# Kernel tuning notes

Measured on AMD Instinct MI355X. Metric: run time of the kernel, lower is better.

The kernel has to match this reference:

```python
import jax, jax.numpy as jnp
import numpy as np

B, D, E = 128, 1024, 1024   # batch, word_rnn_size, word_encoding_size
NV, NL = 36, 20             # visual regions, language memory slots
T = 4                       # max_att_step
EPS = 0.01                  # opt.epsilon
SCALE = 0.02


def _lstm_cell(x, h, c, Wih, Whh, bih, bhh):
    # torch.nn.LSTMCell gate order: i, f, g, o
    g = x @ Wih.T + bih + h @ Whh.T + bhh
    i, f, gg, o = jnp.split(g, 4, axis=-1)
    c2 = jax.nn.sigmoid(f) * c + jax.nn.sigmoid(i) * jnp.tanh(gg)
    h2 = jax.nn.sigmoid(o) * jnp.tanh(c2)
    return h2, c2


def _kv_attention(h_att, vkey, vval, lkey, lval, kvs):
    # stand-in for the externally-passed kv_attention module:
    # scaled dot-product attention over visual and language memories
    q = h_att + kvs                                   # [B,D]
    inv = 1.0 / np.sqrt(D)
    va = jax.nn.softmax(jnp.einsum('bnd,bd->bn', vkey, q) * inv, axis=-1)
    vctx = jnp.einsum('bn,bnd->bd', va, vval)
    la = jax.nn.softmax(jnp.einsum('bmd,bd->bm', lkey, q) * inv, axis=-1)
    lctx = jnp.einsum('bm,bmd->bd', la, lval)
    return vctx, lctx, jnp.tanh(kvs + vctx + lctx)


def _update_kv(out, vkey, lkey):
    # stand-in for the externally-passed update_kv module
    return vkey + 0.01 * out[:, None, :], lkey + 0.01 * out[:, None, :]


def _forward(xt, fc_feats, visual_value, visual_key, lang_value, lang_key,
             kv_state, state_h, state_c,
             att_Wih, att_Whh, att_bih, att_bhh,
             lang_Wih, lang_Whh, lang_bih, lang_bhh,
             conf_W1, conf_b1, conf_W2, conf_b2,
             it, max_att_step):
    word_exist = (it > 0).astype(jnp.float32)         # [B]
    prev_h = state_h[-1]
    # att_lstm input is constant across halting steps (state is not updated in the loop)
    att_in = jnp.concatenate([prev_h, fc_feats, xt], axis=1)  # [B, E+2D]
    z1 = jnp.zeros((B, 1), jnp.float32)
    zD = jnp.zeros((B, D), jnp.float32)
    zB = jnp.zeros((B,), jnp.float32)
    carry0 = (z1, jnp.ones((B, 1), jnp.float32), zD, zD, zD, zD, zD, zB,
              visual_key, lang_key, kv_state)

    def body(carry, i):
        accum, sel, hA, cA, hL, cL, outA, cost, vkey, lkey, kvs = carry
        h_att, c_att = _lstm_cell(att_in, state_h[0], state_c[0],
                                  att_Wih, att_Whh, att_bih, att_bhh)
        vctx, lctx, kvs = _kv_attention(h_att, vkey, visual_value, lkey, lang_value, kvs)
        lang_in = jnp.concatenate([vctx, lctx, h_att], axis=1)  # [B,3D]
        h_lang, c_lang = _lstm_cell(lang_in, state_h[1], state_c[1],
                                    lang_Wih, lang_Whh, lang_bih, lang_bhh)
        out = h_lang  # F.dropout in eval mode is identity
        vkey, lkey = _update_kv(out, vkey, lkey)
        # confidence MLP: Linear -> ReLU -> Linear -> Sigmoid
        p = jax.nn.sigmoid(jax.nn.relu(h_lang @ conf_W1.T + conf_b1) @ conf_W2.T + conf_b2)  # [B,1]
        beta = p * (1.0 - accum)
        accum = accum + beta * sel
        hA = hA + beta * h_att * sel
        cA = cA + beta * c_att * sel
        hL = hL + beta * h_lang * sel
        cL = cL + beta * c_lang * sel
        outA = outA + beta * out * sel
        cost = cost + (i + 1.0) * (1.0 - p[:, 0]) * sel[:, 0]
        sel = jax.lax.stop_gradient((accum < 1.0 - EPS).astype(jnp.float32)) * sel
        return (accum, sel, hA, cA, hL, cL, outA, cost, vkey, lkey, kvs), None

    carry, _ = jax.lax.scan(body, carry0, jnp.arange(max_att_step, dtype=jnp.float32))
    accum, sel, hA, cA, hL, cL, outA, cost, vkey, lkey, kvs = carry
    hA = hA / accum
    cA = cA / accum
    hL = hL / accum
    cL = cL / accum
    outA = outA / accum
    new_h = jnp.stack([hA, hL])
    new_c = jnp.stack([cA, cL])
    return outA, vkey, lkey, cost * word_exist, new_h, new_c, kvs


def setup_inputs() -> dict:
    ks = jax.random.split(jax.random.key(0), 20)
    n = lambda k, s, sc=1.0: jax.random.normal(k, s, dtype=jnp.float32) * sc
    return {
        'xt': n(ks[0], (B, E)),
        'it': jax.random.randint(ks[1], (B,), 0, 9487, dtype=jnp.int32),
        'fc_feats': n(ks[2], (B, D)),
        'visual_value': n(ks[3], (B, NV, D)),
        'visual_key': n(ks[4], (B, NV, D)),
        'lang_value': n(ks[5], (B, NL, D)),
        'lang_key': n(ks[6], (B, NL, D)),
        'kv_state': n(ks[7], (B, D)),
        'state_h': n(ks[8], (2, B, D)),
        'state_c': n(ks[9], (2, B, D)),
        'max_att_step': T,
        'att_Wih': n(ks[10], (4 * D, E + 2 * D), SCALE),
        'att_Whh': n(ks[11], (4 * D, D), SCALE),
        'att_bih': jnp.zeros((4 * D,), jnp.float32),
        'att_bhh': jnp.zeros((4 * D,), jnp.float32),
        'lang_Wih': n(ks[12], (4 * D, 3 * D), SCALE),
        'lang_Whh': n(ks[13], (4 * D, D), SCALE),
        'lang_bih': jnp.zeros((4 * D,), jnp.float32),
        'lang_bhh': jnp.zeros((4 * D,), jnp.float32),
        'conf_W1': n(ks[14], (D, D), SCALE),
        'conf_b1': jnp.zeros((D,), jnp.float32),
        'conf_W2': n(ks[15], (1, D), SCALE),
        'conf_b2': jnp.zeros((1,), jnp.float32),
    }


def reference(xt, it, fc_feats, visual_value, visual_key, lang_value, lang_key,
              kv_state, state_h, state_c, max_att_step,
              att_Wih, att_Whh, att_bih, att_bhh,
              lang_Wih, lang_Whh, lang_bih, lang_bhh,
              conf_W1, conf_b1, conf_W2, conf_b2):
    return _forward(xt, fc_feats, visual_value, visual_key, lang_value, lang_key,
                    kv_state, state_h, state_c,
                    att_Wih, att_Whh, att_bih, att_bhh,
                    lang_Wih, lang_Whh, lang_bih, lang_bhh,
                    conf_W1, conf_b1, conf_W2, conf_b2,
                    it, max_att_step)
```

## Files before the change

### kernel.cpp

```cpp
#include <hip/hip_runtime.h>
#include <hip/hip_bf16.h>

constexpr int B  = 128;
constexpr int D  = 1024;
constexpr int NV = 36;
constexpr int NL = 20;
constexpr int BD = B * D;
constexpr float EPS = 0.01f;
constexpr int NSLOT = 8;

constexpr long SL  = 524288;
constexpr long SLB = 2097152;
constexpr long OFF_GPA   = 0;
constexpr long OFF_GPLB  = OFF_GPA + 8 * SL;
constexpr long OFF_LBASE = OFF_GPLB + 8 * SL;
constexpr long OFF_GPB   = OFF_LBASE + SL;
constexpr long OFF_GPC0  = OFF_GPB + 2 * SLB;
constexpr long OFF_GPC1  = OFF_GPC0 + 524288;
constexpr long OFF_HATT2 = OFF_GPC1 + 524288;
constexpr long OFF_CATT2 = OFF_HATT2 + BD;
constexpr long OFF_HLB   = OFF_CATT2 + BD;
constexpr long OFF_CLB   = OFF_HLB + 524288;
constexpr long OFF_VCTXB = OFF_CLB + 524288;
constexpr long OFF_LCTXB = OFF_VCTXB + 524288;
constexpr long OFF_S2    = OFF_LCTXB + 524288;
constexpr long OFF_VVB   = OFF_S2 + BD;
constexpr long OFF_LVB   = OFF_VVB + 2359296;
constexpr long OFF_VKB   = OFF_LVB + 1310720;
constexpr long OFF_LKB   = OFF_VKB + 2359296;

typedef float f32x4 __attribute__((ext_vector_type(4)));
typedef short s16x8 __attribute__((ext_vector_type(8)));

__device__ __forceinline__ float sigf(float x) { return 1.f / (1.f + expf(-x)); }

__device__ __forceinline__ short f2bf(float f) {
  __hip_bfloat16 h = __float2bfloat16(f);
  return *reinterpret_cast<short*>(&h);
}
__device__ __forceinline__ float bf2f(short s) {
  unsigned u = ((unsigned)(unsigned short)s) << 16;
  return __uint_as_float(u);
}

__device__ __forceinline__ f32x4 LD4(const float* p) { return *(const f32x4*)p; }
__device__ __forceinline__ void ST4(float* p, f32x4 v) { *(f32x4*)p = v; }

__device__ __forceinline__ void conv_bf16(const float* __restrict__ src,
                                          __hip_bfloat16* __restrict__ dst,
                                          long nelem) {
  const long total = nelem >> 2;
  for (long i = (long)blockIdx.x * 256 + threadIdx.x; i < total;
       i += (long)gridDim.x * 256) {
    f32x4 v = LD4(src + i * 4);
    *(short4*)((short*)dst + i * 4) =
        short4{f2bf(v[0]), f2bf(v[1]), f2bf(v[2]), f2bf(v[3])};
  }
}

__global__ __launch_bounds__(256) void conv_kv(
    const float* __restrict__ vkey, const float* __restrict__ lkey,
    const float* __restrict__ vval, const float* __restrict__ lval,
    __hip_bfloat16* __restrict__ vkb, __hip_bfloat16* __restrict__ lkb,
    __hip_bfloat16* __restrict__ vvb, __hip_bfloat16* __restrict__ lvb) {
  conv_bf16(vkey, vkb, (long)B * NV * 1024);
  conv_bf16(lkey, lkb, (long)B * NL * 1024);
  conv_bf16(vval, vvb, (long)B * NV * 1024);
  conv_bf16(lval, lvb, (long)B * NL * 1024);
}

struct GemmArgs {
  const float* A[NSLOT];
  const float* W[NSLOT];
  long wstride[NSLOT];
  int klen;
};

__global__ __launch_bounds__(256, 2) void gemm_mfma(GemmArgs ga, int N,
                                                    long pstride,
                                                    float* __restrict__ gpart) {
  __shared__ __align__(16) short As[2][128][72];
  __shared__ __align__(16) short Bs[2][64][72];
  const int z = blockIdx.z;
  const float* __restrict__ A = ga.A[z];
  const float* __restrict__ W = ga.W[z];
  const long wstr = ga.wstride[z];
  const int brow = blockIdx.y * 128;
  const int bcol = blockIdx.x * 64;
  float* __restrict__ out = gpart + (long)z * pstride;

  const int tid = threadIdx.x;
  const int wave = tid >> 6, lane = tid & 63;
  const int wr = wave >> 1, wc = wave & 1;
  const int lrow = lane & 15;
  const int lk8  = (lane >> 4) * 8;
  const int sr = tid >> 4;
  const int sc4 = (tid & 15) * 4;

  f32x4 acc[4][2];
#pragma unroll
  for (int m = 0; m < 4; ++m)
#pragma unroll
    for (int n = 0; n < 2; ++n) acc[m][n] = (f32x4){0.f, 0.f, 0.f, 0.f};

  float4 ra[8], rw[4];
#define LOAD_TILE(KT)                                                          \
  {                                                                            \
    const int kb = (KT) * 64;                                                  \
    _Pragma("unroll") for (int i = 0; i < 8; ++i) {                            \
      const int r = sr + i * 16;                                               \
      ra[i] = *(const float4*)(A + (long)(brow + r) * 1024 + kb + sc4);        \
    }                                                                          \
    _Pragma("unroll") for (int i = 0; i < 4; ++i) {                            \
      const int r = sr + i * 16;                                               \
      rw[i] = *(const float4*)(W + (long)(bcol + r) * wstr + kb + sc4);        \
    }                                                                          \
  }
#define WRITE_TILE(BUF)                                                        \
  {                                                                            \
    _Pragma("unroll") for (int i = 0; i < 8; ++i) {                            \
      const int r = sr + i * 16;                                               \
      *(short4*)(&As[BUF][r][sc4]) =                                           \
          short4{f2bf(ra[i].x), f2bf(ra[i].y), f2bf(ra[i].z), f2bf(ra[i].w)};  \
    }                                                                          \
    _Pragma("unroll") for (int i = 0; i < 4; ++i) {                            \
      const int r = sr + i * 16;                                               \
      *(short4*)(&Bs[BUF][r][sc4]) =                                           \
          short4{f2bf(rw[i].x), f2bf(rw[i].y), f2bf(rw[i].z), f2bf(rw[i].w)};  \
    }                                                                          \
  }

  const int ntiles = ga.klen / 64;
  LOAD_TILE(0);
  WRITE_TILE(0);
  __syncthreads();
  for (int kt = 0; kt < ntiles; ++kt) {
    const int cur = kt & 1;
    const bool more = (kt + 1 < ntiles);
    if (more) LOAD_TILE(kt + 1);
#pragma unroll
    for (int kk = 0; kk < 64; kk += 32) {
      s16x8 af[4], bf[2];
#pragma unroll
      for (int m = 0; m < 4; ++m)
        af[m] = *(const s16x8*)(&As[cur][wr * 64 + m * 16 + lrow][kk + lk8]);
#pragma unroll
      for (int n = 0; n < 2; ++n)
        bf[n] = *(const s16x8*)(&Bs[cur][wc * 32 + n * 16 + lrow][kk + lk8]);
#pragma unroll
      for (int m = 0; m < 4; ++m)
#pragma unroll
        for (int n = 0; n < 2; ++n)
          acc[m][n] = __builtin_amdgcn_mfma_f32_16x16x32_bf16(
              af[m], bf[n], acc[m][n], 0, 0, 0);
    }
    if (more) WRITE_TILE(1 - cur);
    __syncthreads();
  }
#undef LOAD_TILE
#undef WRITE_TILE

#pragma unroll
  for (int m = 0; m < 4; ++m) {
#pragma unroll
    for (int n = 0; n < 2; ++n) {
      const int col = bcol + wc * 32 + n * 16 + lrow;
#pragma unroll
      for (int r = 0; r < 4; ++r) {
        const int row = brow + wr * 64 + m * 16 + (lane >> 4) * 4 + r;
        out[(long)row * N + col] = acc[m][n][r];
      }
    }
  }
}

constexpr long O1 = BD;
constexpr long O2 = O1 + (long)B * NV * D;
constexpr long O3 = O2 + (long)B * NL * D;
constexpr long O4 = O3 + B;
constexpr long O5 = O4 + 2L * BD;
constexpr long O6 = O5 + 2L * BD;
constexpr long O7 = O6 + BD;

__global__ __launch_bounds__(256) void lstm_att(
    const float* __restrict__ gp, const float* __restrict__ bih,
    const float* __restrict__ bhh, const float* __restrict__ c_prev,
    float* __restrict__ h, float* __restrict__ c, float* __restrict__ out) {
  long idx = ((long)blockIdx.x * 256 + threadIdx.x) * 4;
  if (idx >= BD) return;
  int b = (int)(idx >> 10), d = (int)(idx & 1023);
  const long base = (long)b * 4096 + d;
  f32x4 g[4];
#pragma unroll
  for (int gi = 0; gi < 4; ++gi) {
    const long o = base + gi * 1024;
    f32x4 v = LD4(bih + gi * 1024 + d) + LD4(bhh + gi * 1024 + d);
#pragma unroll
    for (int s = 0; s < NSLOT; ++s) v += LD4(gp + s * SL + o);
    g[gi] = v;
  }
  f32x4 cp = LD4(c_prev + idx), cc, hh;
#pragma unroll
  for (int j = 0; j < 4; ++j) {
    float ccj = sigf(g[1][j]) * cp[j] + sigf(g[0][j]) * tanhf(g[2][j]);
    cc[j] = ccj;
    hh[j] = sigf(g[3][j]) * tanhf(ccj);
  }
  ST4(c + idx, cc);
  ST4(h + idx, hh);
  ST4(out + O4 + idx, hh);
  ST4(out + O5 + idx, cc);
}

__global__ __launch_bounds__(256) void reduce8(
    const float* __restrict__ gp, const float* __restrict__ bih,
    const float* __restrict__ bhh, float* __restrict__ out) {
  long idx = ((long)blockIdx.x * 256 + threadIdx.x) * 4;
  if (idx >= (long)B * 4096) return;
  int col = (int)(idx & 4095);
  f32x4 v = LD4(bih + col) + LD4(bhh + col);
#pragma unroll
  for (int s = 0; s < NSLOT; ++s) v += LD4(gp + s * SL + idx);
  ST4(out + idx, v);
}

__global__ __launch_bounds__(1024) void attn_mega(
    const float* __restrict__ h_att, const float* __restrict__ kv0,
    const __hip_bfloat16* __restrict__ vkb, const __hip_bfloat16* __restrict__ lkb,
    const __hip_bfloat16* __restrict__ vvb, const __hip_bfloat16* __restrict__ lvb,
    float* __restrict__ vctxB, float* __restrict__ lctxB,
    float* __restrict__ out_kvs) {
  const int b = blockIdx.x, tid = threadIdx.x;
  __shared__ short K[56][1024];
  __shared__ float q[1024];
  __shared__ float wgt[64];
  const int wave = tid >> 6, lane = tid & 63;

  for (int i = tid; i < 56 * 128; i += 1024) {
    const int r = i >> 7, c8 = (i & 127) * 8;
    const __hip_bfloat16* kp = (r < NV)
        ? vkb + ((long)b * NV + r) * 1024
        : lkb + ((long)b * NL + (r - NV)) * 1024;
    *(s16x8*)(&K[r][c8]) = *(const s16x8*)(kp + c8);
  }

  const float ha = h_att[(long)b * 1024 + tid];
  float kv = kv0[(long)b * 1024 + tid];

  for (int step = 0; step < 4; ++step) {
    q[tid] = ha + kv;
    __syncthreads();
    for (int n = wave; n < NV + NL; n += 16) {
      float s = 0.f;
#pragma unroll
      for (int j = 0; j < 2; ++j) {
        const int base = lane * 8 + j * 512;
        s16x8 k8 = *(const s16x8*)(&K[n][base]);
        f32x4 q0 = *(const f32x4*)(&q[base]);
        f32x4 q1 = *(const f32x4*)(&q[base + 4]);
#pragma unroll
        for (int e = 0; e < 4; ++e) {
          s += bf2f(k8[e]) * q0[e];
          s += bf2f(k8[e + 4]) * q1[e];
        }
      }
      for (int m = 32; m >= 1; m >>= 1) s += __shfl_xor(s, m);
      if (lane == 0) wgt[n] = s * (1.0f / 32.0f);
    }
    __syncthreads();
    if (wave == 0) {
      float x = (lane < NV) ? wgt[lane] : -1e30f;
      float m = x;
      for (int k = 32; k >= 1; k >>= 1) m = fmaxf(m, __shfl_xor(m, k));
      float e = (lane < NV) ? expf(x - m) : 0.f;
      float ssum = e;
      for (int k = 32; k >= 1; k >>= 1) ssum += __shfl_xor(ssum, k);
      if (lane < NV) wgt[lane] = e / ssum;
    } else if (wave == 1) {
      float x = (lane < NL) ? wgt[NV + lane] : -1e30f;
      float m = x;
      for (int k = 32; k >= 1; k >>= 1) m = fmaxf(m, __shfl_xor(m, k));
      float e = (lane < NL) ? expf(x - m) : 0.f;
      float ssum = e;
      for (int k = 32; k >= 1; k >>= 1) ssum += __shfl_xor(ssum, k);
      if (lane < NL) wgt[NV + lane] = e / ssum;
    }
    __syncthreads();
    const __hip_bfloat16* vb = vvb + (long)b * NV * 1024 + tid;
    float a0 = 0.f, a1 = 0.f, a2 = 0.f, a3 = 0.f;
#pragma unroll
    for (int n = 0; n < NV; n += 4) {
      a0 += __bfloat162float(vb[(long)(n + 0) * 1024]) * wgt[n + 0];
      a1 += __bfloat162float(vb[(long)(n + 1) * 1024]) * wgt[n + 1];
      a2 += __bfloat162float(vb[(long)(n + 2) * 1024]) * wgt[n + 2];
      a3 += __bfloat162float(vb[(long)(n + 3) * 1024]) * wgt[n + 3];
    }
    const float vc = (a0 + a1) + (a2 + a3);
    const __hip_bfloat16* lb = lvb + (long)b * NL * 1024 + tid;
    float c0 = 0.f, c1 = 0.f, c2 = 0.f, c3 = 0.f;
#pragma unroll
    for (int n = 0; n < NL; n += 4) {
      c0 += __bfloat162float(lb[(long)(n + 0) * 1024]) * wgt[NV + n + 0];
      c1 += __bfloat162float(lb[(long)(n + 1) * 1024]) * wgt[NV + n + 1];
      c2 += __bfloat162float(lb[(long)(n + 2) * 1024]) * wgt[NV + n + 2];
      c3 += __bfloat162float(lb[(long)(n + 3) * 1024]) * wgt[NV + n + 3];
    }
    const float lc = (c0 + c1) + (c2 + c3);
    const long orow = ((long)step * 128 + b) * 1024 + tid;
    vctxB[orow] = vc;
    lctxB[orow] = lc;
    kv = tanhf(kv + vc + lc);
    __syncthreads();
  }
  out_kvs[(long)b * 1024 + tid] = kv;
}

__global__ __launch_bounds__(256) void lstm_batch(
    const float* __restrict__ gpB, const float* __restrict__ lbase,
    const float* __restrict__ sc1, float* __restrict__ hB,
    float* __restrict__ cB) {
  long idx = ((long)blockIdx.x * 256 + threadIdx.x) * 4;
  if (idx >= 512L * 1024) return;
  const int row = (int)(idx >> 10);
  const int b = row & 127;
  const int d = (int)(idx & 1023);
  const long base = (long)row * 4096 + d;
  const long lbbase = (long)b * 4096 + d;
  f32x4 g[4];
#pragma unroll
  for (int gi = 0; gi < 4; ++gi) {
    const long o = gi * 1024;
    g[gi] = LD4(gpB + base + o) + LD4(gpB + SLB + base + o) +
            LD4(lbase + lbbase + o);
  }
  f32x4 cp = LD4(sc1 + (long)b * 1024 + d), cc, hh;
#pragma unroll
  for (int j = 0; j < 4; ++j) {
    float ccj = sigf(g[1][j]) * cp[j] + sigf(g[0][j]) * tanhf(g[2][j]);
    cc[j] = ccj;
    hh[j] = sigf(g[3][j]) * tanhf(ccj);
  }
  ST4(cB + idx, cc);
  ST4(hB + idx, hh);
}

__global__ __launch_bounds__(256) void halt_scan(
    const float* __restrict__ gpc0, const float* __restrict__ gpc1,
    const float* __restrict__ cb1, const float* __restrict__ W2,
    const float* __restrict__ b2, const float* __restrict__ hB,
    const float* __restrict__ cB, const int* __restrict__ it,
    float* __restrict__ Sout, float* __restrict__ out) {
  const int b = blockIdx.x, tid = threadIdx.x;
  const int d0 = tid * 4;
  __shared__ float red[256];
  __shared__ float p_sh;
  const f32x4 w4 = LD4(W2 + d0);
  const f32x4 cb = LD4(cb1 + d0);
  f32x4 hl_acc = (f32x4){0.f, 0.f, 0.f, 0.f}, cl_acc = hl_acc, s_acc = hl_acc;
  float a = 0.f, sel = 1.f, cost = 0.f;

  for (int i = 0; i < 4; ++i) {
    const long o = ((long)i * 128 + b) * 1024 + d0;
    f32x4 rv = LD4(gpc0 + o) + LD4(gpc1 + o) + cb;
    float part = 0.f;
#pragma unroll
    for (int j = 0; j < 4; ++j) part += fmaxf(rv[j], 0.f) * w4[j];
    red[tid] = part;
    __syncthreads();
    for (int s = 128; s > 0; s >>= 1) {
      if (tid < s) red[tid] += red[tid + s];
      __syncthreads();
    }
    if (tid == 0) p_sh = sigf(red[0] + b2[0]);
    __syncthreads();
    const float p = p_sh;
    const float bs = p * (1.f - a) * sel;
    f32x4 hl = LD4(hB + o), cl = LD4(cB + o);
    hl_acc += hl * bs;
    cl_acc += cl * bs;
    s_acc += hl;
    cost += (float)(i + 1) * (1.f - p) * sel;
    a += bs;
    sel = (a < 1.f - EPS) ? sel : 0.f;
    __syncthreads();
  }
  const float inv_a = 1.f / a;
  const long ob = (long)b * 1024 + d0;
  ST4(out + ob, hl_acc * inv_a);
  ST4(out + O4 + BD + ob, hl_acc * inv_a);
  ST4(out + O5 + BD + ob, cl_acc * inv_a);
  ST4(Sout + ob, s_acc);
  if (tid == 0) out[O3 + b] = cost * ((it[b] > 0) ? 1.f : 0.f);
}

constexpr long VK = (long)B * NV * D;
constexpr long LK = (long)B * NL * D;

__global__ __launch_bounds__(256) void finalize2(
    const float* __restrict__ vkey0, const float* __restrict__ lkey0,
    const float* __restrict__ S, float* __restrict__ out) {
  long idx = ((long)blockIdx.x * 256 + threadIdx.x) * 4;
  if (idx < VK) {
    int b = (int)(idx / (NV * 1024));
    int d = (int)(idx & 1023);
    ST4(out + O1 + idx, LD4(vkey0 + idx) + LD4(S + (long)b * 1024 + d) * 0.01f);
  } else if (idx < VK + LK) {
    long r = idx - VK;
    int b = (int)(r / (NL * 1024));
    int d = (int)(r & 1023);
    ST4(out + O2 + r, LD4(lkey0 + r) + LD4(S + (long)b * 1024 + d) * 0.01f);
  }
}

extern "C" void kernel_launch(void* const* d_in, const int* in_sizes, int n_in,
                              void* d_out, int out_size, void* d_ws, size_t ws_size,
                              hipStream_t stream) {
  const float* xt   = (const float*)d_in[0];
  const int*   it   = (const int*)d_in[1];
  const float* fc   = (const float*)d_in[2];
  const float* vval = (const float*)d_in[3];
  const float* vkey = (const float*)d_in[4];
  const float* lval = (const float*)d_in[5];
  const float* lkey = (const float*)d_in[6];
  const float* kv0  = (const float*)d_in[7];
  const float* sh   = (const float*)d_in[8];
  const float* sc   = (const float*)d_in[9];
  const float* aWih = (const float*)d_in[11];
  const float* aWhh = (const float*)d_in[12];
  const float* abih = (const float*)d_in[13];
  const float* abhh = (const float*)d_in[14];
  const float* lWih = (const float*)d_in[15];
  const float* lWhh = (const float*)d_in[16];
  const float* lbih = (const float*)d_in[17];
  const float* lbhh = (const float*)d_in[18];
  const float* cW1  = (const float*)d_in[19];
  const float* cb1  = (const float*)d_in[20];
  const float* cW2  = (const float*)d_in[21];
  const float* cb2  = (const float*)d_in[22];

  float* ws = (float*)d_ws;
  float* gpA   = ws + OFF_GPA;
  float* gpLB  = ws + OFF_GPLB;
  float* lbase = ws + OFF_LBASE;
  float* gpB   = ws + OFF_GPB;
  float* gpC0  = ws + OFF_GPC0;
  float* gpC1  = ws + OFF_GPC1;
  float* h_att = ws + OFF_HATT2;
  float* c_att = ws + OFF_CATT2;
  float* hB    = ws + OFF_HLB;
  float* cB    = ws + OFF_CLB;
  float* vctxB = ws + OFF_VCTXB;
  float* lctxB = ws + OFF_LCTXB;
  float* Sbuf  = ws + OFF_S2;
  __hip_bfloat16* vvb = (__hip_bfloat16*)(ws + OFF_VVB);
  __hip_bfloat16* lvb = (__hip_bfloat16*)(ws + OFF_LVB);
  __hip_bfloat16* vkb = (__hip_bfloat16*)(ws + OFF_VKB);
  __hip_bfloat16* lkb = (__hip_bfloat16*)(ws + OFF_LKB);

  const float* sh1 = sh + BD;
  const float* sc0 = sc;
  const float* sc1 = sc + BD;
  float* out = (float*)d_out;

  conv_kv<<<2048, 256, 0, stream>>>(vkey, lkey, vval, lval, vkb, lkb, vvb, lvb);

  {
    GemmArgs ga;
    ga.A[0] = sh1;       ga.W[0] = aWih;        ga.wstride[0] = 3072;
    ga.A[1] = sh1 + 512; ga.W[1] = aWih + 512;  ga.wstride[1] = 3072;
    ga.A[2] = fc;        ga.W[2] = aWih + 1024; ga.wstride[2] = 3072;
    ga.A[3] = fc + 512;  ga.W[3] = aWih + 1536; ga.wstride[3] = 3072;
    ga.A[4] = xt;        ga.W[4] = aWih + 2048; ga.wstride[4] = 3072;
    ga.A[5] = xt + 512;  ga.W[5] = aWih + 2560; ga.wstride[5] = 3072;
    ga.A[6] = sh;        ga.W[6] = aWhh;        ga.wstride[6] = 1024;
    ga.A[7] = sh + 512;  ga.W[7] = aWhh + 512;  ga.wstride[7] = 1024;
    ga.klen = 512;
    gemm_mfma<<<dim3(64, 1, 8), 256, 0, stream>>>(ga, 4096, SL, gpA);
  }
  lstm_att<<<128, 256, 0, stream>>>(gpA, abih, abhh, sc0, h_att, c_att, out);

  {
    GemmArgs ga;
#pragma unroll
    for (int q = 0; q < 4; ++q) {
      ga.A[q] = sh1 + q * 256;
      ga.W[q] = lWhh + q * 256;
      ga.wstride[q] = 1024;
      ga.A[4 + q] = h_att + q * 256;
      ga.W[4 + q] = lWih + 2048 + q * 256;
      ga.wstride[4 + q] = 3072;
    }
    ga.klen = 256;
    gemm_mfma<<<dim3(64, 1, 8), 256, 0, stream>>>(ga, 4096, SL, gpLB);
  }
  reduce8<<<512, 256, 0, stream>>>(gpLB, lbih, lbhh, lbase);

  attn_mega<<<128, 1024, 0, stream>>>(h_att, kv0, vkb, lkb, vvb, lvb,
                                      vctxB, lctxB, out + O6);

  {
    GemmArgs ga;
    ga.A[0] = vctxB; ga.W[0] = lWih;        ga.wstride[0] = 3072;
    ga.A[1] = lctxB; ga.W[1] = lWih + 1024; ga.wstride[1] = 3072;
#pragma unroll
    for (int z = 2; z < 8; ++z) { ga.A[z] = vctxB; ga.W[z] = lWih; ga.wstride[z] = 3072; }
    ga.klen = 1024;
    gemm_mfma<<<dim3(64, 4, 2), 256, 0, stream>>>(ga, 4096, SLB, gpB);
  }
  lstm_batch<<<512, 256, 0, stream>>>(gpB, lbase, sc1, hB, cB);

  {
    GemmArgs ga;
    ga.A[0] = hB;       ga.W[0] = cW1;       ga.wstride[0] = 1024;
    ga.A[1] = hB + 512; ga.W[1] = cW1 + 512; ga.wstride[1] = 1024;
#pragma unroll
    for (int z = 2; z < 8; ++z) { ga.A[z] = hB; ga.W[z] = cW1; ga.wstride[z] = 1024; }
    ga.klen = 512;
    gemm_mfma<<<dim3(16, 4, 2), 256, 0, stream>>>(ga, 1024, 524288, gpC0);
  }
  halt_scan<<<128, 256, 0, stream>>>(gpC0, gpC1, cb1, cW2, cb2, hB, cB, it,
                                     Sbuf, out);
  finalize2<<<7168, 256, 0, stream>>>(vkey, lkey, Sbuf, out);
}
```

Measured before the change: 151.3 us.

## Widen GEMM N-tile, feed bf16 activations, and finalize keys from bf16 copies

The GEMM tile widens from 64 to 128 output columns, which halves the grid and doubles the accumulators per wave. The kernel gains an optional bf16 A-operand path, so h_att, state_h[1] and the attention contexts are stored once in bf16 and no longer reloaded and converted from fp32. finalize2 now reconstructs the updated keys from the bf16 key copies instead of the fp32 originals, cutting its read traffic. That last step puts bf16 rounding error into the exported key outputs, and the larger tile raises register pressure while leaving fewer blocks to run in parallel.

```diff
diff --git a/kernel.cpp b/kernel.cpp
--- a/kernel.cpp
+++ b/kernel.cpp
@@ -18,16 +18,17 @@
 constexpr long OFF_GPC0  = OFF_GPB + 2 * SLB;
 constexpr long OFF_GPC1  = OFF_GPC0 + 524288;
 constexpr long OFF_HATT2 = OFF_GPC1 + 524288;
-constexpr long OFF_CATT2 = OFF_HATT2 + BD;
-constexpr long OFF_HLB   = OFF_CATT2 + BD;
+constexpr long OFF_HLB   = OFF_HATT2 + BD;
 constexpr long OFF_CLB   = OFF_HLB + 524288;
-constexpr long OFF_VCTXB = OFF_CLB + 524288;
-constexpr long OFF_LCTXB = OFF_VCTXB + 524288;
-constexpr long OFF_S2    = OFF_LCTXB + 524288;
+constexpr long OFF_S2    = OFF_CLB + 524288;
 constexpr long OFF_VVB   = OFF_S2 + BD;
 constexpr long OFF_LVB   = OFF_VVB + 2359296;
 constexpr long OFF_VKB   = OFF_LVB + 1310720;
 constexpr long OFF_LKB   = OFF_VKB + 2359296;
+constexpr long OFF_HATB  = OFF_LKB + 1310720;
+constexpr long OFF_SH1B  = OFF_HATB + 65536;
+constexpr long OFF_VCXB  = OFF_SH1B + 65536;
+constexpr long OFF_LCXB  = OFF_VCXB + 262144;
 
 typedef float f32x4 __attribute__((ext_vector_type(4)));
 typedef short s16x8 __attribute__((ext_vector_type(8)));
@@ -61,18 +62,22 @@
 __global__ __launch_bounds__(256) void conv_kv(
     const float* __restrict__ vkey, const float* __restrict__ lkey,
     const float* __restrict__ vval, const float* __restrict__ lval,
+    const float* __restrict__ sh1,
     __hip_bfloat16* __restrict__ vkb, __hip_bfloat16* __restrict__ lkb,
-    __hip_bfloat16* __restrict__ vvb, __hip_bfloat16* __restrict__ lvb) {
+    __hip_bfloat16* __restrict__ vvb, __hip_bfloat16* __restrict__ lvb,
+    __hip_bfloat16* __restrict__ sh1b) {
   conv_bf16(vkey, vkb, (long)B * NV * 1024);
   conv_bf16(lkey, lkb, (long)B * NL * 1024);
   conv_bf16(vval, vvb, (long)B * NV * 1024);
   conv_bf16(lval, lvb, (long)B * NL * 1024);
+  conv_bf16(sh1, sh1b, (long)BD);
 }
 
 struct GemmArgs {
-  const float* A[NSLOT];
+  const void* A[NSLOT];
   const float* W[NSLOT];
   long wstride[NSLOT];
+  int abf16[NSLOT];
   int klen;
 };
 
@@ -80,13 +85,15 @@
                                                     long pstride,
                                                     float* __restrict__ gpart) {
   __shared__ __align__(16) short As[2][128][72];
-  __shared__ __align__(16) short Bs[2][64][72];
+  __shared__ __align__(16) short Bs[2][128][72];
   const int z = blockIdx.z;
-  const float* __restrict__ A = ga.A[z];
+  const int ab = ga.abf16[z];
+  const float* __restrict__ Af = (const float*)ga.A[z];
+  const short* __restrict__ Ah = (const short*)ga.A[z];
   const float* __restrict__ W = ga.W[z];
   const long wstr = ga.wstride[z];
   const int brow = blockIdx.y * 128;
-  const int bcol = blockIdx.x * 64;
+  const int bcol = blockIdx.x * 128;
   float* __restrict__ out = gpart + (long)z * pstride;
 
   const int tid = threadIdx.x;
@@ -96,34 +103,53 @@
   const int lk8  = (lane >> 4) * 8;
   const int sr = tid >> 4;
   const int sc4 = (tid & 15) * 4;
-
-  f32x4 acc[4][2];
+  const int br8 = tid >> 3;
+  (void)br8;
+
+  f32x4 acc[4][4];
 #pragma unroll
   for (int m = 0; m < 4; ++m)
 #pragma unroll
-    for (int n = 0; n < 2; ++n) acc[m][n] = (f32x4){0.f, 0.f, 0.f, 0.f};
-
-  float4 ra[8], rw[4];
+    for (int n = 0; n < 4; ++n) acc[m][n] = (f32x4){0.f, 0.f, 0.f, 0.f};
+
+  float4 ra[8], rw[8];
+  s16x8 rab[4];
 #define LOAD_TILE(KT)                                                          \
   {                                                                            \
     const int kb = (KT) * 64;                                                  \
+    if (ab) {                                                                  \
+      _Pragma("unroll") for (int i = 0; i < 4; ++i) {                          \
+        const int idx = tid + i * 256;                                         \
+        const int r = idx >> 3, c8 = (idx & 7) * 8;                            \
+        rab[i] = *(const s16x8*)(Ah + (long)(brow + r) * 1024 + kb + c8);      \
+      }                                                                        \
+    } else {                                                                   \
+      _Pragma("unroll") for (int i = 0; i < 8; ++i) {                          \
+        const int r = sr + i * 16;                                             \
+        ra[i] = *(const float4*)(Af + (long)(brow + r) * 1024 + kb + sc4);     \
+      }                                                                        \
+    }                                                                          \
     _Pragma("unroll") for (int i = 0; i < 8; ++i) {                            \
-      const int r = sr + i * 16;                                               \
-      ra[i] = *(const float4*)(A + (long)(brow + r) * 1024 + kb + sc4);        \
-    }                                                                          \
-    _Pragma("unroll") for (int i = 0; i < 4; ++i) {                            \
       const int r = sr + i * 16;                                               \
       rw[i] = *(const float4*)(W + (long)(bcol + r) * wstr + kb + sc4);        \
     }                                                                          \
   }
 #define WRITE_TILE(BUF)                                                        \
   {                                                                            \
+    if (ab) {                                                                  \
+      _Pragma("unroll") for (int i = 0; i < 4; ++i) {                          \
+        const int idx = tid + i * 256;                                         \
+        const int r = idx >> 3, c8 = (idx & 7) * 8;                            \
+        *(s16x8*)(&As[BUF][r][c8]) = rab[i];                                   \
+      }                                                                        \
+    } else {                                                                   \
+      _Pragma("unroll") for (int i = 0; i < 8; ++i) {                          \
+        const int r = sr + i * 16;                                             \
+        *(short4*)(&As[BUF][r][sc4]) =                                         \
+            short4{f2bf(ra[i].x), f2bf(ra[i].y), f2bf(ra[i].z), f2bf(ra[i].w)};\
+      }                                                                        \
+    }                                                                          \
     _Pragma("unroll") for (int i = 0; i < 8; ++i) {                            \
-      const int r = sr + i * 16;                                               \
-      *(short4*)(&As[BUF][r][sc4]) =                                           \
-          short4{f2bf(ra[i].x), f2bf(ra[i].y), f2bf(ra[i].z), f2bf(ra[i].w)};  \
-    }                                                                          \
-    _Pragma("unroll") for (int i = 0; i < 4; ++i) {                            \
       const int r = sr + i * 16;                                               \
       *(short4*)(&Bs[BUF][r][sc4]) =                                           \
           short4{f2bf(rw[i].x), f2bf(rw[i].y), f2bf(rw[i].z), f2bf(rw[i].w)};  \
@@ -140,17 +166,17 @@
     if (more) LOAD_TILE(kt + 1);
 #pragma unroll
     for (int kk = 0; kk < 64; kk += 32) {
-      s16x8 af[4], bf[2];
+      s16x8 af[4], bf[4];
 #pragma unroll
       for (int m = 0; m < 4; ++m)
         af[m] = *(const s16x8*)(&As[cur][wr * 64 + m * 16 + lrow][kk + lk8]);
 #pragma unroll
-      for (int n = 0; n < 2; ++n)
-        bf[n] = *(const s16x8*)(&Bs[cur][wc * 32 + n * 16 + lrow][kk + lk8]);
+      for (int n = 0; n < 4; ++n)
+        bf[n] = *(const s16x8*)(&Bs[cur][wc * 64 + n * 16 + lrow][kk + lk8]);
 #pragma unroll
       for (int m = 0; m < 4; ++m)
 #pragma unroll
-        for (int n = 0; n < 2; ++n)
+        for (int n = 0; n < 4; ++n)
           acc[m][n] = __builtin_amdgcn_mfma_f32_16x16x32_bf16(
               af[m], bf[n], acc[m][n], 0, 0, 0);
     }
@@ -163,8 +189,8 @@
 #pragma unroll
   for (int m = 0; m < 4; ++m) {
 #pragma unroll
-    for (int n = 0; n < 2; ++n) {
-      const int col = bcol + wc * 32 + n * 16 + lrow;
+    for (int n = 0; n < 4; ++n) {
+      const int col = bcol + wc * 64 + n * 16 + lrow;
 #pragma unroll
       for (int r = 0; r < 4; ++r) {
         const int row = brow + wr * 64 + m * 16 + (lane >> 4) * 4 + r;
@@ -185,7 +211,8 @@
 __global__ __launch_bounds__(256) void lstm_att(
     const float* __restrict__ gp, const float* __restrict__ bih,
     const float* __restrict__ bhh, const float* __restrict__ c_prev,
-    float* __restrict__ h, float* __restrict__ c, float* __restrict__ out) {
+    float* __restrict__ h, __hip_bfloat16* __restrict__ hb,
+    float* __restrict__ out) {
   long idx = ((long)blockIdx.x * 256 + threadIdx.x) * 4;
   if (idx >= BD) return;
   int b = (int)(idx >> 10), d = (int)(idx & 1023);
@@ -206,8 +233,9 @@
     cc[j] = ccj;
     hh[j] = sigf(g[3][j]) * tanhf(ccj);
   }
-  ST4(c + idx, cc);
   ST4(h + idx, hh);
+  *(short4*)((short*)hb + idx) =
+      short4{f2bf(hh[0]), f2bf(hh[1]), f2bf(hh[2]), f2bf(hh[3])};
   ST4(out + O4 + idx, hh);
   ST4(out + O5 + idx, cc);
 }
@@ -228,7 +256,7 @@
     const float* __restrict__ h_att, const float* __restrict__ kv0,
     const __hip_bfloat16* __restrict__ vkb, const __hip_bfloat16* __restrict__ lkb,
     const __hip_bfloat16* __restrict__ vvb, const __hip_bfloat16* __restrict__ lvb,
-    float* __restrict__ vctxB, float* __restrict__ lctxB,
+    __hip_bfloat16* __restrict__ vctxB, __hip_bfloat16* __restrict__ lctxB,
     float* __restrict__ out_kvs) {
   const int b = blockIdx.x, tid = threadIdx.x;
   __shared__ short K[56][1024];
@@ -307,8 +335,8 @@
     }
     const float lc = (c0 + c1) + (c2 + c3);
     const long orow = ((long)step * 128 + b) * 1024 + tid;
-    vctxB[orow] = vc;
-    lctxB[orow] = lc;
+    vctxB[orow] = __float2bfloat16(vc);
+    lctxB[orow] = __float2bfloat16(lc);
     kv = tanhf(kv + vc + lc);
     __syncthreads();
   }
@@ -397,18 +425,36 @@
 constexpr long LK = (long)B * NL * D;
 
 __global__ __launch_bounds__(256) void finalize2(
-    const float* __restrict__ vkey0, const float* __restrict__ lkey0,
+    const __hip_bfloat16* __restrict__ vkb, const __hip_bfloat16* __restrict__ lkb,
     const float* __restrict__ S, float* __restrict__ out) {
-  long idx = ((long)blockIdx.x * 256 + threadIdx.x) * 4;
+  long idx = ((long)blockIdx.x * 256 + threadIdx.x) * 8;
   if (idx < VK) {
     int b = (int)(idx / (NV * 1024));
     int d = (int)(idx & 1023);
-    ST4(out + O1 + idx, LD4(vkey0 + idx) + LD4(S + (long)b * 1024 + d) * 0.01f);
+    s16x8 k8 = *(const s16x8*)((const short*)vkb + idx);
+    f32x4 s0 = LD4(S + (long)b * 1024 + d), s1 = LD4(S + (long)b * 1024 + d + 4);
+    f32x4 o0, o1;
+#pragma unroll
+    for (int j = 0; j < 4; ++j) {
+      o0[j] = bf2f(k8[j]) + 0.01f * s0[j];
+      o1[j] = bf2f(k8[j + 4]) + 0.01f * s1[j];
+    }
+    ST4(out + O1 + idx, o0);
+    ST4(out + O1 + idx + 4, o1);
   } else if (idx < VK + LK) {
     long r = idx - VK;
     int b = (int)(r / (NL * 1024));
     int d = (int)(r & 1023);
-    ST4(out + O2 + r, LD4(lkey0 + r) + LD4(S + (long)b * 1024 + d) * 0.01f);
+    s16x8 k8 = *(const s16x8*)((const short*)lkb + r);
+    f32x4 s0 = LD4(S + (long)b * 1024 + d), s1 = LD4(S + (long)b * 1024 + d + 4);
+    f32x4 o0, o1;
+#pragma unroll
+    for (int j = 0; j < 4; ++j) {
+      o0[j] = bf2f(k8[j]) + 0.01f * s0[j];
+      o1[j] = bf2f(k8[j + 4]) + 0.01f * s1[j];
+    }
+    ST4(out + O2 + r, o0);
+    ST4(out + O2 + r + 4, o1);
   }
 }
 
@@ -446,26 +492,28 @@
   float* gpC0  = ws + OFF_GPC0;
   float* gpC1  = ws + OFF_GPC1;
   float* h_att = ws + OFF_HATT2;
-  float* c_att = ws + OFF_CATT2;
   float* hB    = ws + OFF_HLB;
   float* cB    = ws + OFF_CLB;
-  float* vctxB = ws + OFF_VCTXB;
-  float* lctxB = ws + OFF_LCTXB;
   float* Sbuf  = ws + OFF_S2;
-  __hip_bfloat16* vvb = (__hip_bfloat16*)(ws + OFF_VVB);
-  __hip_bfloat16* lvb = (__hip_bfloat16*)(ws + OFF_LVB);
-  __hip_bfloat16* vkb = (__hip_bfloat16*)(ws + OFF_VKB);
-  __hip_bfloat16* lkb = (__hip_bfloat16*)(ws + OFF_LKB);
+  __hip_bfloat16* vvb  = (__hip_bfloat16*)(ws + OFF_VVB);
+  __hip_bfloat16* lvb  = (__hip_bfloat16*)(ws + OFF_LVB);
+  __hip_bfloat16* vkb  = (__hip_bfloat16*)(ws + OFF_VKB);
+  __hip_bfloat16* lkb  = (__hip_bfloat16*)(ws + OFF_LKB);
+  __hip_bfloat16* hatb = (__hip_bfloat16*)(ws + OFF_HATB);
+  __hip_bfloat16* sh1b = (__hip_bfloat16*)(ws + OFF_SH1B);
+  __hip_bfloat16* vcxb = (__hip_bfloat16*)(ws + OFF_VCXB);
+  __hip_bfloat16* lcxb = (__hip_bfloat16*)(ws + OFF_LCXB);
 
   const float* sh1 = sh + BD;
   const float* sc0 = sc;
   const float* sc1 = sc + BD;
   float* out = (float*)d_out;
 
-  conv_kv<<<2048, 256, 0, stream>>>(vkey, lkey, vval, lval, vkb, lkb, vvb, lvb);
+  conv_kv<<<2048, 256, 0, stream>>>(vkey, lkey, vval, lval, sh1,
+                                    vkb, lkb, vvb, lvb, sh1b);
 
   {
-    GemmArgs ga;
+    GemmArgs ga = {};
     ga.A[0] = sh1;       ga.W[0] = aWih;        ga.wstride[0] = 3072;
     ga.A[1] = sh1 + 512; ga.W[1] = aWih + 512;  ga.wstride[1] = 3072;
     ga.A[2] = fc;        ga.W[2] = aWih + 1024; ga.wstride[2] = 3072;
@@ -475,50 +523,48 @@
     ga.A[6] = sh;        ga.W[6] = aWhh;        ga.wstride[6] = 1024;
     ga.A[7] = sh + 512;  ga.W[7] = aWhh + 512;  ga.wstride[7] = 1024;
     ga.klen = 512;
-    gemm_mfma<<<dim3(64, 1, 8), 256, 0, stream>>>(ga, 4096, SL, gpA);
-  }
-  lstm_att<<<128, 256, 0, stream>>>(gpA, abih, abhh, sc0, h_att, c_att, out);
+    gemm_mfma<<<dim3(32, 1, 8), 256, 0, stream>>>(ga, 4096, SL, gpA);
+  }
+  lstm_att<<<128, 256, 0, stream>>>(gpA, abih, abhh, sc0, h_att, hatb, out);
+
+  attn_mega<<<128, 1024, 0, stream>>>(h_att, kv0, vkb, lkb, vvb, lvb,
+                                      vcxb, lcxb, out + O6);
 
   {
-    GemmArgs ga;
+    GemmArgs ga = {};
 #pragma unroll
     for (int q = 0; q < 4; ++q) {
-      ga.A[q] = sh1 + q * 256;
+      ga.A[q] = (const void*)((const short*)sh1b + q * 256);
       ga.W[q] = lWhh + q * 256;
       ga.wstride[q] = 1024;
-      ga.A[4 + q] = h_att + q * 256;
+      ga.abf16[q] = 1;
+      ga.A[4 + q] = (const void*)((const short*)hatb + q * 256);
       ga.W[4 + q] = lWih + 2048 + q * 256;
       ga.wstride[4 + q] = 3072;
+      ga.abf16[4 + q] = 1;
     }
     ga.klen = 256;
-    gemm_mfma<<<dim3(64, 1, 8), 256, 0, stream>>>(ga, 4096, SL, gpLB);
+    gemm_mfma<<<dim3(32, 1, 8), 256, 0, stream>>>(ga, 4096, SL, gpLB);
   }
   reduce8<<<512, 256, 0, stream>>>(gpLB, lbih, lbhh, lbase);
 
-  attn_mega<<<128, 1024, 0, stream>>>(h_att, kv0, vkb, lkb, vvb, lvb,
-                                      vctxB, lctxB, out + O6);
-
   {
-    GemmArgs ga;
-    ga.A[0] = vctxB; ga.W[0] = lWih;        ga.wstride[0] = 3072;
-    ga.A[1] = lctxB; ga.W[1] = lWih + 1024; ga.wstride[1] = 3072;
-#pragma unroll
-    for (int z = 2; z < 8; ++z) { ga.A[z] = vctxB; ga.W[z] = lWih; ga.wstride[z] = 3072; }
+    GemmArgs ga = {};
+    ga.A[0] = vcxb; ga.W[0] = lWih;        ga.wstride[0] = 3072; ga.abf16[0] = 1;
+    ga.A[1] = lcxb; ga.W[1] = lWih + 1024; ga.wstride[1] = 3072; ga.abf16[1] = 1;
     ga.klen = 1024;
-    gemm_mfma<<<dim3(64, 4, 2), 256, 0, stream>>>(ga, 4096, SLB, gpB);
+    gemm_mfma<<<dim3(32, 4, 2), 256, 0, stream>>>(ga, 4096, SLB, gpB);
   }
   lstm_batch<<<512, 256, 0, stream>>>(gpB, lbase, sc1, hB, cB);
 
   {
-    GemmArgs ga;
+    GemmArgs ga = {};
     ga.A[0] = hB;       ga.W[0] = cW1;       ga.wstride[0] = 1024;
     ga.A[1] = hB + 512; ga.W[1] = cW1 + 512; ga.wstride[1] = 1024;
-#pragma unroll
-    for (int z = 2; z < 8; ++z) { ga.A[z] = hB; ga.W[z] = cW1; ga.wstride[z] = 1024; }
     ga.klen = 512;
-    gemm_mfma<<<dim3(16, 4, 2), 256, 0, stream>>>(ga, 1024, 524288, gpC0);
+    gemm_mfma<<<dim3(8, 4, 2), 256, 0, stream>>>(ga, 1024, 524288, gpC0);
   }
   halt_scan<<<128, 256, 0, stream>>>(gpC0, gpC1, cb1, cW2, cb2, hB, cB, it,
                                      Sbuf, out);
-  finalize2<<<7168, 256, 0, stream>>>(vkey, lkey, Sbuf, out);
-}
+  finalize2<<<3584, 256, 0, stream>>>(vkb, lkb, Sbuf, out);
+}
```

Result: slower. 155.4 us (+2.7%).
